# Kernel tuning notes

Measured on AMD Instinct MI355X. Metric: run time of the kernel, lower is better.

The kernel has to match this reference:

```python
import jax
import jax.numpy as jnp
from jax import lax
import numpy as np

B, T, IN, H, K = 8, 4096, 512, 512, 2


def setup_inputs() -> dict:
    key = jax.random.key(0)
    k = jax.random.split(key, 5)
    scale_w0 = 1.0 / np.sqrt(IN * K)
    scale_w1 = 1.0 / np.sqrt(H * K)
    return {
        "x": jax.random.normal(k[0], (B, T, IN), jnp.float32),
        "w0": jax.random.normal(k[1], (3 * H, IN, K), jnp.float32) * scale_w0,
        "b0": jax.random.normal(k[2], (3 * H,), jnp.float32) * scale_w0,
        "w1": jax.random.normal(k[3], (3 * H, H, K), jnp.float32) * scale_w1,
        "b1": jax.random.normal(k[4], (3 * H,), jnp.float32) * scale_w1,
    }


def _qrnn_layer(x, w, b):
    # x: [B, T, C]; w: [3H, C, K]; causal conv (left pad K-1), matching
    # torch padding=K-1 then slicing off the last K-1 timesteps.
    xc = jnp.transpose(x, (0, 2, 1))  # [B, C, T]
    conv = lax.conv_general_dilated(
        xc, w, window_strides=(1,), padding=[(K - 1, 0)],
        dimension_numbers=("NCH", "OIH", "NCH"))
    conv = conv + b[None, :, None]
    conv = jnp.transpose(conv, (0, 2, 1))  # [B, T, 3H]
    z, f, o = jnp.split(conv, 3, axis=-1)
    z = jnp.tanh(z)
    f = jax.nn.sigmoid(f)
    o = jax.nn.sigmoid(o)

    def step(h, zfo):
        zt, ft, ot = zfo
        h = ft * h + (1.0 - ft) * zt  # fo-pool recurrence
        return h, ot * h

    h0 = jnp.zeros((x.shape[0], z.shape[-1]), x.dtype)
    hT, outs = lax.scan(
        step, h0,
        (jnp.swapaxes(z, 0, 1), jnp.swapaxes(f, 0, 1), jnp.swapaxes(o, 0, 1)))
    return jnp.swapaxes(outs, 0, 1), hT  # [B, T, H], [B, H]


def reference(x, w0, b0, w1, b1):
    out, h0 = _qrnn_layer(x, w0, b0)
    out, h1 = _qrnn_layer(out, w1, b1)
    return out, h0, h1
```

## Files before the change

kernel.cpp:

```cpp
#include <hip/hip_runtime.h>
#include <cstdint>

#define B_ 8
#define T_ 4096
#define TP1 4097
#define IN_ 512
#define H_ 512
#define N3H 1536
#define KD 1024
#define CHUNKS 64
#define CLEN 64

typedef __attribute__((ext_vector_type(4))) float floatx4;
typedef __attribute__((ext_vector_type(4))) float f4;
typedef __attribute__((ext_vector_type(8))) short short8;
typedef __attribute__((ext_vector_type(4))) unsigned short us4;
typedef __attribute__((ext_vector_type(4))) _Float16 h4;

__device__ __forceinline__ unsigned short f2bf(float v){
  unsigned int u = __float_as_uint(v);
  unsigned int r = (u + 0x7fffu + ((u >> 16) & 1u)) >> 16;
  return (unsigned short)r;
}
__device__ __forceinline__ float sigm(float x){
  return __builtin_amdgcn_rcpf(1.f + __expf(-x));
}
__device__ __forceinline__ float tanhf_(float x){ return 2.f*sigm(2.f*x) - 1.f; }

#define GLLS(src, dst) __builtin_amdgcn_global_load_lds( \
    (const __attribute__((address_space(1))) void*)(src), \
    (__attribute__((address_space(3))) void*)(dst), 16, 0, 0)

__global__ void cast_pad_kernel(const float* __restrict__ x, unsigned short* __restrict__ xpad){
  int64_t i = (int64_t)blockIdx.x*256 + threadIdx.x;
  const int64_t total = (int64_t)B_*TP1*(IN_/4);
  if (i >= total) return;
  int cg = (int)(i & 127);
  int64_t r = i >> 7;
  int t = (int)(r % TP1);
  int b = (int)(r / TP1);
  us4 o;
  if (t == 0){ o = (us4){0,0,0,0}; }
  else {
    f4 v = *(const f4*)(x + ((int64_t)b*T_ + (t-1))*IN_ + cg*4);
    #pragma unroll
    for (int u=0;u<4;++u) o[u] = f2bf(v[u]);
  }
  *(us4*)(xpad + r*IN_ + cg*4) = o;
}

__global__ void wt_kernel(const float* __restrict__ wA, unsigned short* __restrict__ wtA,
                          const float* __restrict__ wB, unsigned short* __restrict__ wtB){
  int i = blockIdx.x*256 + threadIdx.x;
  if (i >= N3H*512) return;
  const float* w = blockIdx.y ? wB : wA;
  unsigned short* wt = blockIdx.y ? wtB : wtA;
  int ci = i & 511;
  int o = i >> 9;
  const float* wp = w + (int64_t)o*KD + ci*2;
  wt[(int64_t)o*KD + ci]       = f2bf(wp[0]);
  wt[(int64_t)o*KD + 512 + ci] = f2bf(wp[1]);
}

__global__ __launch_bounds__(256) void gemm_kernel(
    const unsigned short* __restrict__ A, const unsigned short* __restrict__ W,
    const float* __restrict__ bias, _Float16* __restrict__ C){
  __shared__ unsigned short As[128*32];
  __shared__ unsigned short Bs[128*32];
  const int tid = threadIdx.x;
  const int lane = tid & 63;
  const int wave = tid >> 6;
  const int bid = blockIdx.x;
  const int xcd = bid & 7;
  const int kb  = bid >> 3;
  const int colt = kb % 12;
  const int rowt = (kb / 12) * 8 + xcd;
  const int m0 = rowt * 128;
  const int n0 = colt * 128;
  const int bb = m0 / T_;
  const int act = n0 >> 9;
  const unsigned short* aSrc = A + (int64_t)(m0 + bb + (tid>>2))*IN_ + (tid&3)*8;
  const unsigned short* bSrc = W + (int64_t)(n0 + (tid>>2))*KD + (tid&3)*8;
  unsigned short* aDst = As + tid*8;
  unsigned short* bDst = Bs + tid*8;
  const int wm = wave & 1;
  const int wn = wave >> 1;
  const int l16 = lane & 15;
  const int quad = lane >> 4;
  floatx4 acc[4][4];
  #pragma unroll
  for (int i=0;i<4;i++)
    #pragma unroll
    for (int j=0;j<4;j++) acc[i][j] = (floatx4){0.f,0.f,0.f,0.f};
  const unsigned short* aLds = As + (wm*64 + l16)*32 + quad*8;
  const unsigned short* bLds = Bs + (wn*64 + l16)*32 + quad*8;

  for (int kk = 0; kk < KD; kk += 32){
    __syncthreads();
    GLLS(aSrc + kk,           aDst);
    GLLS(aSrc + 64*IN_ + kk,  aDst + 2048);
    GLLS(bSrc + kk,           bDst);
    GLLS(bSrc + 64*KD + kk,   bDst + 2048);
    __syncthreads();
    short8 af[4], bfr[4];
    #pragma unroll
    for (int i=0;i<4;i++) af[i] = *(const short8*)(aLds + i*16*32);
    #pragma unroll
    for (int j=0;j<4;j++) bfr[j] = *(const short8*)(bLds + j*16*32);
    #pragma unroll
    for (int i=0;i<4;i++)
      #pragma unroll
      for (int j=0;j<4;j++)
        acc[i][j] = __builtin_amdgcn_mfma_f32_16x16x32_bf16(af[i], bfr[j], acc[i][j], 0, 0, 0);
  }
  float bv[4];
  #pragma unroll
  for (int j=0;j<4;j++) bv[j] = bias[n0 + wn*64 + j*16 + l16];
  #pragma unroll
  for (int i=0;i<4;i++){
    int row = m0 + wm*64 + i*16 + quad*4;
    #pragma unroll
    for (int j=0;j<4;j++){
      int col = n0 + wn*64 + j*16 + l16;
      _Float16* cp = C + (int64_t)row*N3H + col;
      #pragma unroll
      for (int r=0;r<4;r++){
        float v = acc[i][j][r] + bv[j];
        v = (act == 0) ? tanhf_(v) : sigm(v);
        cp[(int64_t)r*N3H] = (_Float16)v;
      }
    }
  }
}

__global__ void scan_phase1(const _Float16* __restrict__ conv,
                            float* __restrict__ carA, float* __restrict__ carB){
  int q = blockIdx.x*256 + threadIdx.x;
  int chg = q & 127;
  int bq = (q >> 7) & 7;
  int c  = q >> 10;
  int ch = chg*4;
  f4 Aa = {1.f,1.f,1.f,1.f}, Bb = {0.f,0.f,0.f,0.f};
  const _Float16* p = conv + ((int64_t)bq*T_ + c*CLEN)*N3H + ch;
  for (int g=0; g<CLEN/8; ++g){
    h4 zb[8], fb[8];
    #pragma unroll
    for (int u=0;u<8;++u){
      zb[u] = *(const h4*)(p + (int64_t)u*N3H);
      fb[u] = *(const h4*)(p + (int64_t)u*N3H + 512);
    }
    #pragma unroll
    for (int u=0;u<8;++u){
      #pragma unroll
      for (int v=0;v<4;++v){
        float fv = (float)fb[u][v];
        float zv = (float)zb[u][v];
        Aa[v] *= fv;
        Bb[v] = fv*Bb[v] + (1.f-fv)*zv;
      }
    }
    p += (int64_t)8*N3H;
  }
  *(f4*)(carA + (int64_t)q*4) = Aa;
  *(f4*)(carB + (int64_t)q*4) = Bb;
}

__global__ void scan_phase2(const float* __restrict__ carA, const float* __restrict__ carB,
                            float* __restrict__ hstart, float* __restrict__ hT){
  int q = blockIdx.x*256 + threadIdx.x;
  float h = 0.f;
  for (int c=0;c<CHUNKS;++c){
    int64_t idx = (int64_t)c*4096 + q;
    hstart[idx] = h;
    h = carA[idx]*h + carB[idx];
  }
  hT[q] = h;
}

template<int LAYER>
__global__ void scan_phase3(const _Float16* __restrict__ conv,
                            const float* __restrict__ hstart, unsigned short* __restrict__ xpad,
                            float* __restrict__ outf){
  int q = blockIdx.x*256 + threadIdx.x;
  int chg = q & 127;
  int bq = (q >> 7) & 7;
  int c  = q >> 10;
  int ch = chg*4;
  f4 h;
  #pragma unroll
  for (int v=0;v<4;++v) h[v] = hstart[(int64_t)c*4096 + bq*512 + ch + v];
  const _Float16* p = conv + ((int64_t)bq*T_ + c*CLEN)*N3H + ch;
  int t = c*CLEN;
  for (int g=0; g<CLEN/8; ++g){
    h4 zb[8], fb[8], ob[8];
    #pragma unroll
    for (int u=0;u<8;++u){
      zb[u] = *(const h4*)(p + (int64_t)u*N3H);
      fb[u] = *(const h4*)(p + (int64_t)u*N3H + 512);
      ob[u] = *(const h4*)(p + (int64_t)u*N3H + 1024);
    }
    #pragma unroll
    for (int u=0;u<8;++u){
      if (LAYER == 0){
        us4 ov4;
        #pragma unroll
        for (int v=0;v<4;++v){
          float fv = (float)fb[u][v];
          h[v] = fv*h[v] + (1.f-fv)*(float)zb[u][v];
          ov4[v] = f2bf((float)ob[u][v]*h[v]);
        }
        *(us4*)(xpad + ((int64_t)bq*TP1 + t+u + 1)*IN_ + ch) = ov4;
      } else {
        f4 of4;
        #pragma unroll
        for (int v=0;v<4;++v){
          float fv = (float)fb[u][v];
          h[v] = fv*h[v] + (1.f-fv)*(float)zb[u][v];
          of4[v] = (float)ob[u][v]*h[v];
        }
        *(f4*)(outf + ((int64_t)bq*T_ + t+u)*H_ + ch) = of4;
      }
    }
    t += 8; p += (int64_t)8*N3H;
  }
}

extern "C" void kernel_launch(void* const* d_in, const int* in_sizes, int n_in,
                              void* d_out, int out_size, void* d_ws, size_t ws_size,
                              hipStream_t stream){
  const float* x  = (const float*)d_in[0];
  const float* w0 = (const float*)d_in[1];
  const float* b0 = (const float*)d_in[2];
  const float* w1 = (const float*)d_in[3];
  const float* b1 = (const float*)d_in[4];
  float* out = (float*)d_out;

  char* ws = (char*)d_ws;
  size_t off = 0;
  auto alloc = [&](size_t bytes)->char*{
    char* p = ws + off; off = (off + bytes + 255) & ~(size_t)255; return p; };
  unsigned short* xpad = (unsigned short*)alloc((size_t)B_*TP1*IN_*2);
  unsigned short* Wt0  = (unsigned short*)alloc((size_t)N3H*KD*2);
  unsigned short* Wt1  = (unsigned short*)alloc((size_t)N3H*KD*2);
  _Float16* conv = (_Float16*)alloc((size_t)B_*T_*N3H*2);
  float* carA = (float*)alloc((size_t)CHUNKS*4096*4);
  float* carB = (float*)alloc((size_t)CHUNKS*4096*4);
  float* hst  = (float*)alloc((size_t)CHUNKS*4096*4);
  if (off > ws_size) return;

  float* out_main = out;
  float* h0 = out + (int64_t)B_*T_*H_;
  float* h1 = h0 + B_*H_;

  const int64_t padN = (int64_t)B_*TP1*(IN_/4);
  cast_pad_kernel<<<(int)((padN + 255)/256), 256, 0, stream>>>(x, xpad);
  dim3 wgrid((N3H*512 + 255)/256, 2);
  wt_kernel<<<wgrid, 256, 0, stream>>>(w0, Wt0, w1, Wt1);

  const int ggrid = (N3H/128) * ((B_*T_)/128);
  const int sgrid = (CHUNKS*8*128) / 256;
  gemm_kernel<<<ggrid, 256, 0, stream>>>(xpad, Wt0, b0, conv);
  scan_phase1<<<sgrid, 256, 0, stream>>>(conv, carA, carB);
  scan_phase2<<<16, 256, 0, stream>>>(carA, carB, hst, h0);
  scan_phase3<0><<<sgrid, 256, 0, stream>>>(conv, hst, xpad, nullptr);

  gemm_kernel<<<ggrid, 256, 0, stream>>>(xpad, Wt1, b1, conv);
  scan_phase1<<<sgrid, 256, 0, stream>>>(conv, carA, carB);
  scan_phase2<<<16, 256, 0, stream>>>(carA, carB, hst, h1);
  scan_phase3<1><<<sgrid, 256, 0, stream>>>(conv, hst, nullptr, out_main);
}
```

Baseline: 458.0 us.

## Fuse three-phase chunked scan into single kernel with grid-wide atomic barrier

Replaces the three scan kernels (chunk reduce, serial carry propagation, chunk replay) with one fused kernel. Each block computes its chunk's prefix coefficients, caches per-step (A,B) pairs in LDS as fp16, waits at a spin barrier built on an atomic counter, then derives its starting state by folding the carries of earlier chunks. The sequence is split into two halves so 512 blocks can all be resident at once. This removes a kernel launch, the re-read of z/f from global memory and the serial phase2 pass. The costs are a grid barrier that depends on every block being co-resident, redundant carry folding of up to 31 steps per thread, and fp16 rounding of the cumulative A and B values, which reduces accuracy.

```diff
diff --git a/kernel.cpp b/kernel.cpp
--- a/kernel.cpp
+++ b/kernel.cpp
@@ -8,14 +8,14 @@
 #define H_ 512
 #define N3H 1536
 #define KD 1024
-#define CHUNKS 64
+#define HCH 32
 #define CLEN 64
 
 typedef __attribute__((ext_vector_type(4))) float floatx4;
 typedef __attribute__((ext_vector_type(4))) float f4;
 typedef __attribute__((ext_vector_type(8))) short short8;
 typedef __attribute__((ext_vector_type(4))) unsigned short us4;
-typedef __attribute__((ext_vector_type(4))) _Float16 h4;
+typedef __attribute__((ext_vector_type(2))) _Float16 h2;
 
 __device__ __forceinline__ unsigned short f2bf(float v){
   unsigned int u = __float_as_uint(v);
@@ -31,9 +31,11 @@
     (const __attribute__((address_space(1))) void*)(src), \
     (__attribute__((address_space(3))) void*)(dst), 16, 0, 0)
 
-__global__ void cast_pad_kernel(const float* __restrict__ x, unsigned short* __restrict__ xpad){
+__global__ void cast_pad_kernel(const float* __restrict__ x, unsigned short* __restrict__ xpad,
+                                int* __restrict__ ctrs){
   int64_t i = (int64_t)blockIdx.x*256 + threadIdx.x;
   const int64_t total = (int64_t)B_*TP1*(IN_/4);
+  if (i < 4) ctrs[i] = 0;
   if (i >= total) return;
   int cg = (int)(i & 127);
   int64_t r = i >> 7;
@@ -133,96 +135,71 @@
   }
 }
 
-__global__ void scan_phase1(const _Float16* __restrict__ conv,
-                            float* __restrict__ carA, float* __restrict__ carB){
-  int q = blockIdx.x*256 + threadIdx.x;
-  int chg = q & 127;
-  int bq = (q >> 7) & 7;
-  int c  = q >> 10;
-  int ch = chg*4;
-  f4 Aa = {1.f,1.f,1.f,1.f}, Bb = {0.f,0.f,0.f,0.f};
-  const _Float16* p = conv + ((int64_t)bq*T_ + c*CLEN)*N3H + ch;
+template<int LAYER, int HALF>
+__global__ __launch_bounds__(256) void scan_fused(
+    const _Float16* __restrict__ conv,
+    const float* __restrict__ hin,
+    float* __restrict__ hout,
+    float* __restrict__ carA, float* __restrict__ carB,
+    unsigned short* __restrict__ xpad, float* __restrict__ outf,
+    int* __restrict__ ctr){
+  __shared__ h2 AB[CLEN*256];
+  const int tid = threadIdx.x;
+  const int bid = blockIdx.x;
+  const int c  = bid >> 4;
+  const int bq = (bid >> 1) & 7;
+  const int hc = bid & 1;
+  const int ch = hc*256 + tid;
+  const int t0 = HALF*2048 + c*CLEN;
+  const _Float16* p = conv + ((int64_t)bq*T_ + t0)*N3H + ch;
+  float Aa = 1.f, Bb = 0.f;
   for (int g=0; g<CLEN/8; ++g){
-    h4 zb[8], fb[8];
+    float zv[8], fv[8];
     #pragma unroll
     for (int u=0;u<8;++u){
-      zb[u] = *(const h4*)(p + (int64_t)u*N3H);
-      fb[u] = *(const h4*)(p + (int64_t)u*N3H + 512);
+      zv[u] = (float)p[(int64_t)(g*8+u)*N3H];
+      fv[u] = (float)p[(int64_t)(g*8+u)*N3H + 512];
     }
     #pragma unroll
     for (int u=0;u<8;++u){
-      #pragma unroll
-      for (int v=0;v<4;++v){
-        float fv = (float)fb[u][v];
-        float zv = (float)zb[u][v];
-        Aa[v] *= fv;
-        Bb[v] = fv*Bb[v] + (1.f-fv)*zv;
-      }
-    }
-    p += (int64_t)8*N3H;
-  }
-  *(f4*)(carA + (int64_t)q*4) = Aa;
-  *(f4*)(carB + (int64_t)q*4) = Bb;
-}
-
-__global__ void scan_phase2(const float* __restrict__ carA, const float* __restrict__ carB,
-                            float* __restrict__ hstart, float* __restrict__ hT){
-  int q = blockIdx.x*256 + threadIdx.x;
-  float h = 0.f;
-  for (int c=0;c<CHUNKS;++c){
-    int64_t idx = (int64_t)c*4096 + q;
-    hstart[idx] = h;
-    h = carA[idx]*h + carB[idx];
-  }
-  hT[q] = h;
-}
-
-template<int LAYER>
-__global__ void scan_phase3(const _Float16* __restrict__ conv,
-                            const float* __restrict__ hstart, unsigned short* __restrict__ xpad,
-                            float* __restrict__ outf){
-  int q = blockIdx.x*256 + threadIdx.x;
-  int chg = q & 127;
-  int bq = (q >> 7) & 7;
-  int c  = q >> 10;
-  int ch = chg*4;
-  f4 h;
-  #pragma unroll
-  for (int v=0;v<4;++v) h[v] = hstart[(int64_t)c*4096 + bq*512 + ch + v];
-  const _Float16* p = conv + ((int64_t)bq*T_ + c*CLEN)*N3H + ch;
-  int t = c*CLEN;
+      Aa *= fv[u];
+      Bb = fv[u]*Bb + (1.f-fv[u])*zv[u];
+      h2 ab; ab[0] = (_Float16)Aa; ab[1] = (_Float16)Bb;
+      AB[(g*8+u)*256 + tid] = ab;
+    }
+  }
+  carA[(c*8+bq)*512 + ch] = Aa;
+  carB[(c*8+bq)*512 + ch] = Bb;
+  __syncthreads();
+  if (tid == 0){
+    __threadfence();
+    atomicAdd(ctr, 1);
+    int it = 0;
+    while (__hip_atomic_load(ctr, __ATOMIC_RELAXED, __HIP_MEMORY_SCOPE_AGENT) < 512
+           && it < 100000000) ++it;
+  }
+  __syncthreads();
+  __threadfence();
+  float h0 = (HALF == 1) ? hin[bq*512 + ch] : 0.f;
+  for (int cc=0; cc<c; ++cc)
+    h0 = carA[(cc*8+bq)*512 + ch]*h0 + carB[(cc*8+bq)*512 + ch];
+  const _Float16* po = conv + ((int64_t)bq*T_ + t0)*N3H + 1024 + ch;
   for (int g=0; g<CLEN/8; ++g){
-    h4 zb[8], fb[8], ob[8];
+    float ov[8];
+    #pragma unroll
+    for (int u=0;u<8;++u) ov[u] = (float)po[(int64_t)(g*8+u)*N3H];
     #pragma unroll
     for (int u=0;u<8;++u){
-      zb[u] = *(const h4*)(p + (int64_t)u*N3H);
-      fb[u] = *(const h4*)(p + (int64_t)u*N3H + 512);
-      ob[u] = *(const h4*)(p + (int64_t)u*N3H + 1024);
-    }
-    #pragma unroll
-    for (int u=0;u<8;++u){
-      if (LAYER == 0){
-        us4 ov4;
-        #pragma unroll
-        for (int v=0;v<4;++v){
-          float fv = (float)fb[u][v];
-          h[v] = fv*h[v] + (1.f-fv)*(float)zb[u][v];
-          ov4[v] = f2bf((float)ob[u][v]*h[v]);
-        }
-        *(us4*)(xpad + ((int64_t)bq*TP1 + t+u + 1)*IN_ + ch) = ov4;
-      } else {
-        f4 of4;
-        #pragma unroll
-        for (int v=0;v<4;++v){
-          float fv = (float)fb[u][v];
-          h[v] = fv*h[v] + (1.f-fv)*(float)zb[u][v];
-          of4[v] = (float)ob[u][v]*h[v];
-        }
-        *(f4*)(outf + ((int64_t)bq*T_ + t+u)*H_ + ch) = of4;
-      }
-    }
-    t += 8; p += (int64_t)8*N3H;
-  }
+      int t = g*8 + u;
+      h2 ab = AB[t*256 + tid];
+      float hv = (float)ab[0]*h0 + (float)ab[1];
+      float oh = ov[u]*hv;
+      if (LAYER == 0) xpad[((int64_t)bq*TP1 + t0 + t + 1)*IN_ + ch] = f2bf(oh);
+      else            outf[((int64_t)bq*T_ + t0 + t)*H_ + ch] = oh;
+    }
+  }
+  if (c == HCH-1)
+    hout[bq*512 + ch] = Aa*h0 + Bb;
 }
 
 extern "C" void kernel_launch(void* const* d_in, const int* in_sizes, int n_in,
@@ -243,9 +220,13 @@
   unsigned short* Wt0  = (unsigned short*)alloc((size_t)N3H*KD*2);
   unsigned short* Wt1  = (unsigned short*)alloc((size_t)N3H*KD*2);
   _Float16* conv = (_Float16*)alloc((size_t)B_*T_*N3H*2);
-  float* carA = (float*)alloc((size_t)CHUNKS*4096*4);
-  float* carB = (float*)alloc((size_t)CHUNKS*4096*4);
-  float* hst  = (float*)alloc((size_t)CHUNKS*4096*4);
+  float* carA[4]; float* carB[4];
+  for (int i=0;i<4;++i){
+    carA[i] = (float*)alloc((size_t)HCH*8*512*4);
+    carB[i] = (float*)alloc((size_t)HCH*8*512*4);
+  }
+  float* hcarry = (float*)alloc((size_t)B_*H_*4);
+  int* ctrs = (int*)alloc(4*sizeof(int));
   if (off > ws_size) return;
 
   float* out_main = out;
@@ -253,19 +234,16 @@
   float* h1 = h0 + B_*H_;
 
   const int64_t padN = (int64_t)B_*TP1*(IN_/4);
-  cast_pad_kernel<<<(int)((padN + 255)/256), 256, 0, stream>>>(x, xpad);
+  cast_pad_kernel<<<(int)((padN + 255)/256), 256, 0, stream>>>(x, xpad, ctrs);
   dim3 wgrid((N3H*512 + 255)/256, 2);
   wt_kernel<<<wgrid, 256, 0, stream>>>(w0, Wt0, w1, Wt1);
 
   const int ggrid = (N3H/128) * ((B_*T_)/128);
-  const int sgrid = (CHUNKS*8*128) / 256;
   gemm_kernel<<<ggrid, 256, 0, stream>>>(xpad, Wt0, b0, conv);
-  scan_phase1<<<sgrid, 256, 0, stream>>>(conv, carA, carB);
-  scan_phase2<<<16, 256, 0, stream>>>(carA, carB, hst, h0);
-  scan_phase3<0><<<sgrid, 256, 0, stream>>>(conv, hst, xpad, nullptr);
+  scan_fused<0,0><<<512, 256, 0, stream>>>(conv, nullptr, hcarry, carA[0], carB[0], xpad, nullptr, ctrs+0);
+  scan_fused<0,1><<<512, 256, 0, stream>>>(conv, hcarry, h0,     carA[1], carB[1], xpad, nullptr, ctrs+1);
 
   gemm_kernel<<<ggrid, 256, 0, stream>>>(xpad, Wt1, b1, conv);
-  scan_phase1<<<sgrid, 256, 0, stream>>>(conv, carA, carB);
-  scan_phase2<<<16, 256, 0, stream>>>(carA, carB, hst, h1);
-  scan_phase3<1><<<sgrid, 256, 0, stream>>>(conv, hst, nullptr, out_main);
-}
+  scan_fused<1,0><<<512, 256, 0, stream>>>(conv, nullptr, hcarry, carA[2], carB[2], nullptr, out_main, ctrs+2);
+  scan_fused<1,1><<<512, 256, 0, stream>>>(conv, hcarry, h1,     carA[3], carB[3], nullptr, out_main, ctrs+3);
+}
```

Result: slower. 700.0 us (+52.8%).

## Fuse carry-propagation scan into phase3 and use shorter chunks

Applied to the files above, without the earlier changes.

Removes the separate serial scan_phase2 kernel. Each phase3 thread now recomputes its starting state by folding all preceding chunk carries itself, and the last chunk writes the final hidden state. The chunk count doubles to 128 with length 32, which gives phase1 and phase3 more threads and a shorter serial loop. In exchange, later chunks do redundant carry reads whose count grows linearly with the chunk index, and the kernels become load-imbalanced.

```diff
diff --git a/kernel.cpp b/kernel.cpp
--- a/kernel.cpp
+++ b/kernel.cpp
@@ -8,8 +8,8 @@
 #define H_ 512
 #define N3H 1536
 #define KD 1024
-#define CHUNKS 64
-#define CLEN 64
+#define CHUNKS 128
+#define CLEN 32
 
 typedef __attribute__((ext_vector_type(4))) float floatx4;
 typedef __attribute__((ext_vector_type(4))) float f4;
@@ -165,30 +165,41 @@
   *(f4*)(carB + (int64_t)q*4) = Bb;
 }
 
-__global__ void scan_phase2(const float* __restrict__ carA, const float* __restrict__ carB,
-                            float* __restrict__ hstart, float* __restrict__ hT){
-  int q = blockIdx.x*256 + threadIdx.x;
-  float h = 0.f;
-  for (int c=0;c<CHUNKS;++c){
-    int64_t idx = (int64_t)c*4096 + q;
-    hstart[idx] = h;
-    h = carA[idx]*h + carB[idx];
-  }
-  hT[q] = h;
-}
-
 template<int LAYER>
 __global__ void scan_phase3(const _Float16* __restrict__ conv,
-                            const float* __restrict__ hstart, unsigned short* __restrict__ xpad,
-                            float* __restrict__ outf){
+                            const float* __restrict__ carA, const float* __restrict__ carB,
+                            unsigned short* __restrict__ xpad, float* __restrict__ outf,
+                            float* __restrict__ hT){
   int q = blockIdx.x*256 + threadIdx.x;
   int chg = q & 127;
   int bq = (q >> 7) & 7;
   int c  = q >> 10;
   int ch = chg*4;
-  f4 h;
-  #pragma unroll
-  for (int v=0;v<4;++v) h[v] = hstart[(int64_t)c*4096 + bq*512 + ch + v];
+  f4 h = {0.f,0.f,0.f,0.f};
+  {
+    int cc = 0;
+    while (cc + 8 <= c){
+      f4 av[8], bv[8];
+      #pragma unroll
+      for (int u=0;u<8;++u){
+        int64_t idx = (int64_t)((cc+u)*8 + bq)*512 + ch;
+        av[u] = *(const f4*)(carA + idx);
+        bv[u] = *(const f4*)(carB + idx);
+      }
+      #pragma unroll
+      for (int u=0;u<8;++u)
+        #pragma unroll
+        for (int v=0;v<4;++v) h[v] = av[u][v]*h[v] + bv[u][v];
+      cc += 8;
+    }
+    for (; cc < c; ++cc){
+      int64_t idx = (int64_t)(cc*8 + bq)*512 + ch;
+      f4 a = *(const f4*)(carA + idx);
+      f4 b = *(const f4*)(carB + idx);
+      #pragma unroll
+      for (int v=0;v<4;++v) h[v] = a[v]*h[v] + b[v];
+    }
+  }
   const _Float16* p = conv + ((int64_t)bq*T_ + c*CLEN)*N3H + ch;
   int t = c*CLEN;
   for (int g=0; g<CLEN/8; ++g){
@@ -223,6 +234,8 @@
     }
     t += 8; p += (int64_t)8*N3H;
   }
+  if (c == CHUNKS-1)
+    *(f4*)(hT + bq*512 + ch) = h;
 }
 
 extern "C" void kernel_launch(void* const* d_in, const int* in_sizes, int n_in,
@@ -245,7 +258,6 @@
   _Float16* conv = (_Float16*)alloc((size_t)B_*T_*N3H*2);
   float* carA = (float*)alloc((size_t)CHUNKS*4096*4);
   float* carB = (float*)alloc((size_t)CHUNKS*4096*4);
-  float* hst  = (float*)alloc((size_t)CHUNKS*4096*4);
   if (off > ws_size) return;
 
   float* out_main = out;
@@ -261,11 +273,9 @@
   const int sgrid = (CHUNKS*8*128) / 256;
   gemm_kernel<<<ggrid, 256, 0, stream>>>(xpad, Wt0, b0, conv);
   scan_phase1<<<sgrid, 256, 0, stream>>>(conv, carA, carB);
-  scan_phase2<<<16, 256, 0, stream>>>(carA, carB, hst, h0);
-  scan_phase3<0><<<sgrid, 256, 0, stream>>>(conv, hst, xpad, nullptr);
+  scan_phase3<0><<<sgrid, 256, 0, stream>>>(conv, carA, carB, xpad, nullptr, h0);
 
   gemm_kernel<<<ggrid, 256, 0, stream>>>(xpad, Wt1, b1, conv);
   scan_phase1<<<sgrid, 256, 0, stream>>>(conv, carA, carB);
-  scan_phase2<<<16, 256, 0, stream>>>(carA, carB, hst, h1);
-  scan_phase3<1><<<sgrid, 256, 0, stream>>>(conv, hst, nullptr, out_main);
-}
+  scan_phase3<1><<<sgrid, 256, 0, stream>>>(conv, carA, carB, nullptr, out_main, h1);
+}
```

Measured after the change: 468.9 us. 1.02x slower.
